# Kernel tuning notes

Measured on AMD Instinct MI355X. Metric: run time of the kernel, lower is better.

Reference implementation:

```python
import jax, jax.numpy as jnp
import numpy as np

S, B, T = 128, 1024, 96
E, H, HH, ATT = 64, 200, 100, 200
ACT, FLD = 32, 8
V_SRC, N_PROD, V_PRIM, N_FLD = 20000, 101, 10000, 64
DEC_IN = ACT + ATT + FLD + H  # 440


def setup_inputs() -> dict:
    key = jax.random.key(0)
    ks = jax.random.split(key, 24)
    rn = lambda k, shp: jax.random.normal(k, shp, dtype=jnp.float32) * 0.05
    sentences = jax.random.randint(ks[0], (S, B), 0, V_SRC)
    is_prod = jax.random.randint(ks[1], (T, B), 0, 2).astype(jnp.int32)
    prod_ids = jax.random.randint(ks[2], (T, B), 0, N_PROD)
    prim_ids = jax.random.randint(ks[3], (T, B), 0, V_PRIM)
    field_ids = jax.random.randint(ks[4], (T, B), 0, N_FLD)
    pt = jax.random.randint(ks[5], (T, B), 0, T)
    parent_t = jnp.minimum(pt, jnp.maximum(jnp.arange(T)[:, None] - 1, 0))  # parent < t
    return {
        'sentences': sentences, 'is_prod': is_prod, 'prod_ids': prod_ids,
        'prim_ids': prim_ids, 'field_ids': field_ids, 'parent_t': parent_t,
        'src_emb': rn(ks[6], (V_SRC, E)),
        'actprod_emb': rn(ks[7], (N_PROD, ACT)),
        'prim_emb': rn(ks[8], (V_PRIM, ACT)),
        'field_emb': rn(ks[9], (N_FLD, FLD)),
        'Wih_f': rn(ks[10], (4 * HH, E)), 'Whh_f': rn(ks[11], (4 * HH, HH)), 'b_f': rn(ks[12], (4 * HH,)),
        'Wih_b': rn(ks[13], (4 * HH, E)), 'Whh_b': rn(ks[14], (4 * HH, HH)), 'b_b': rn(ks[15], (4 * HH,)),
        'Wih_d': rn(ks[16], (4 * H, DEC_IN)), 'Whh_d': rn(ks[17], (4 * H, H)), 'b_d': rn(ks[18], (4 * H,)),
        'W_attn': rn(ks[19], (H, H)),
        'W_av': rn(ks[20], (ATT, 2 * H)),
    }


def _lstm_cell(z, c):
    i, f, g, o = jnp.split(z, 4, axis=-1)  # torch gate order i,f,g,o
    c = jax.nn.sigmoid(f) * c + jax.nn.sigmoid(i) * jnp.tanh(g)
    h = jax.nn.sigmoid(o) * jnp.tanh(c)
    return h, c


def _lstm_dir(x_emb, Wih, Whh, b, reverse):
    # x_emb: [S,B,E]; precompute input projections once
    xw = jnp.einsum('sbe,he->sbh', x_emb, Wih) + b
    nb = x_emb.shape[1]
    hh = Whh.shape[1]
    init = (jnp.zeros((nb, hh), x_emb.dtype), jnp.zeros((nb, hh), x_emb.dtype))
    def step(carry, xw_t):
        h, c = carry
        h, c = _lstm_cell(xw_t + h @ Whh.T, c)
        return (h, c), h
    (hT, cT), hs = jax.lax.scan(step, init, xw, reverse=reverse)
    return hs, hT, cT


def _forward(sentences, is_prod, prod_ids, prim_ids, field_ids, parent_t,
             src_emb, actprod_emb, prim_emb, field_emb,
             Wih_f, Whh_f, b_f, Wih_b, Whh_b, b_b,
             Wih_d, Whh_d, b_d, W_attn, W_av):
    nb = sentences.shape[1]
    nt = is_prod.shape[0]
    emb = src_emb[sentences]                       # [S,B,E]
    hs_f, hTf, cTf = _lstm_dir(emb, Wih_f, Whh_f, b_f, False)
    hs_b, hTb, cTb = _lstm_dir(emb, Wih_b, Whh_b, b_b, True)
    enc = jnp.concatenate([hs_f, hs_b], -1).transpose(1, 0, 2)   # [B,S,H]
    enc_att = enc @ W_attn.T                                     # [B,S,H]
    # replicate torch h0.view(-1, H) on [2,B,HH]
    h = jnp.stack([hTf, hTb]).reshape(-1, H)
    c = jnp.stack([cTf, cTb]).reshape(-1, H)
    Hbuf = jnp.zeros((nt, nb, H), enc.dtype)
    s_att0 = jnp.zeros((nb, ATT), enc.dtype)
    barange = jnp.arange(nb)

    def dec_step(carry, xs):
        h, c, s_att, Hbuf = carry
        t, ip, pid, prid, fid, ptid = xs
        a_tm1 = jnp.where(ip[:, None] == 1, actprod_emb[pid], prim_emb[prid])  # [B,32]
        nft = field_emb[fid]                                                   # [B,8]
        parent = Hbuf[ptid, barange]                                           # [B,H] irregular gather
        inp = jnp.concatenate([a_tm1, s_att, nft, parent], axis=-1)           # [B,440]
        inp = jnp.where(t > 0, inp, jnp.zeros_like(inp))
        h, c = _lstm_cell(inp @ Wih_d.T + h @ Whh_d.T + b_d, c)
        aw = jax.nn.softmax(jnp.einsum('bsh,bh->bs', enc_att, h), axis=-1)
        ctx = jnp.einsum('bs,bsh->bh', aw, enc)
        s_att = jnp.tanh(jnp.concatenate([ctx, h], axis=1) @ W_av.T)
        Hbuf = Hbuf.at[t].set(h)
        return (h, c, s_att, Hbuf), s_att

    xs = (jnp.arange(nt), is_prod, prod_ids, prim_ids, field_ids, parent_t)
    _, att_vecs = jax.lax.scan(dec_step, (h, c, s_att0, Hbuf), xs)
    return att_vecs  # [T,B,ATT]


def reference(sentences, is_prod, prod_ids, prim_ids, field_ids, parent_t,
              src_emb, actprod_emb, prim_emb, field_emb,
              Wih_f, Whh_f, b_f, Wih_b, Whh_b, b_b,
              Wih_d, Whh_d, b_d, W_attn, W_av):
    return _forward(sentences, is_prod, prod_ids, prim_ids, field_ids, parent_t,
                    src_emb, actprod_emb, prim_emb, field_emb,
                    Wih_f, Whh_f, b_f, Wih_b, Whh_b, b_b,
                    Wih_d, Whh_d, b_d, W_attn, W_av)
```

## Files before the change

### kernel.cpp

```cpp
#include <hip/hip_runtime.h>

#define S_LEN 128
#define B_N   1024
#define T_LEN 96
#define E_DIM 64
#define HH    100
#define H_DIM 200
#define ACT_D 32
#define FLD_D 8
#define ATT_D 200
#define DEC_IN 440
#define KTOT  640
#define G4H   800
#define G4HH  400
#define KH_PAD 224
#define KC_PAD 416
#define NCOL_PAD 208
#define EK_ROWS 208
#define XA_LD 648
#define HG_LD 232
#define CAT_LD 424

typedef unsigned int  u32;
typedef unsigned short u16;
typedef _Float16 f16;
typedef _Float16 f16x8 __attribute__((ext_vector_type(8)));
typedef _Float16 f16x4 __attribute__((ext_vector_type(4)));
typedef float    f32x4 __attribute__((ext_vector_type(4)));

#define MFMA16(a,b,c) __builtin_amdgcn_mfma_f32_16x16x32_f16((a),(b),(c),0,0,0)

static __device__ __forceinline__ float lo_bf(u32 u){ union{u32 i; float f;}v; v.i = u<<16; return v.f; }
static __device__ __forceinline__ float hi_bf(u32 u){ union{u32 i; float f;}v; v.i = u & 0xffff0000u; return v.f; }
static __device__ __forceinline__ float sigf(float x){
  x = fminf(30.f, fmaxf(-30.f, x));
  return 1.f/(1.f + __expf(-x));
}
static __device__ __forceinline__ float tanhf_(float x){
  x = fminf(15.f, fmaxf(-15.f, x));
  float e = __expf(-2.f*x);
  return (1.f - e)/(1.f + e);
}

static __device__ __forceinline__ u16 f2bf(float f){
  union{float f; u32 i;} v; v.f = f;
  u32 r = v.i + 0x7fffu + ((v.i >> 16) & 1u);
  return (u16)(r >> 16);
}
__global__ void k_prep(u16* __restrict__ dst, const float* __restrict__ src,
                       int K, int C, int sk, int sc)
{
  int idx = blockIdx.x*256 + threadIdx.x;
  if (idx >= K*C) return;
  int k = idx / C, c = idx - k*C;
  dst[(size_t)(k>>2)*(4*C) + 4*c + (k&3)] = f2bf(src[(size_t)k*sk + (size_t)c*sc]);
}

__global__ void k_pack16(f16* __restrict__ dst, const float* __restrict__ src,
                         int Kld, int koff, int C, int K, int sk, int sc)
{
  int idx = blockIdx.x*256 + threadIdx.x;
  if (idx >= C*K) return;
  int c = idx / K, k = idx - c*K;
  dst[(size_t)c*Kld + koff + k] = (f16)src[(size_t)k*sk + (size_t)c*sc];
}

__global__ void k_zf16(f16* __restrict__ dst, int n)
{
  int idx = blockIdx.x*256 + threadIdx.x;
  if (idx < n) dst[idx] = (f16)0.f;
}

__global__ __launch_bounds__(256) void k_transpose(
    const f16* __restrict__ enc_sk, f16* __restrict__ enc_ks)
{
  __shared__ f16 ld[H_DIM][136];
  const int b = blockIdx.x, tid = threadIdx.x;
  const f16* src = enc_sk + (size_t)b*S_LEN*H_DIM;
  for (int idx = tid; idx < S_LEN*(H_DIM/4); idx += 256) {
    int s = idx / (H_DIM/4), jc = idx - s*(H_DIM/4);
    f16x4 v = *(const f16x4*)(src + (size_t)s*H_DIM + 4*jc);
    #pragma unroll
    for (int i = 0; i < 4; ++i) ld[4*jc + i][s] = v[i];
  }
  __syncthreads();
  f16* dst = enc_ks + (size_t)b*EK_ROWS*S_LEN;
  for (int idx = tid; idx < H_DIM*(S_LEN/8); idx += 256) {
    int k = idx / (S_LEN/8), so = idx - k*(S_LEN/8);
    f16x8 v;
    #pragma unroll
    for (int i = 0; i < 8; ++i) v[i] = ld[k][8*so + i];
    *(f16x8*)(dst + (size_t)k*S_LEN + 8*so) = v;
  }
}

__global__ __launch_bounds__(512) void k_attgemm(
    const f16* __restrict__ enc_sk, const f16* __restrict__ wattnT,
    f16* __restrict__ enc_att)
{
  __shared__ alignas(16) f16 et[S_LEN][KH_PAD];
  const int b = blockIdx.x, tid = threadIdx.x;
  const int lane = tid & 63, wid = tid >> 6;
  const int arow = lane & 15, aoff = (lane >> 4) * 8;
  const f16* src = enc_sk + (size_t)b*S_LEN*H_DIM;
  for (int idx = tid; idx < S_LEN*(H_DIM/8); idx += 512) {
    int s = idx / (H_DIM/8), jo = idx - s*(H_DIM/8);
    *(f16x8*)&et[s][8*jo] = *(const f16x8*)(src + (size_t)s*H_DIM + 8*jo);
  }
  for (int idx = tid; idx < S_LEN*3; idx += 512) {
    int s = idx / 3, jo = idx - s*3;
    *(f16x8*)&et[s][H_DIM + 8*jo] = (f16x8){0,0,0,0,0,0,0,0};
  }
  __syncthreads();
  f16x8 af[7];
  #pragma unroll
  for (int kk = 0; kk < 7; ++kk)
    af[kk] = *(const f16x8*)&et[wid*16 + arow][kk*32 + aoff];
  f16* dstb = enc_att + (size_t)b*EK_ROWS*S_LEN;
  for (int tt = 0; tt < 13; ++tt) {
    int c = tt*16 + arow;
    f32x4 acc = {0.f,0.f,0.f,0.f};
    const f16* p = wattnT + (size_t)c*KH_PAD + aoff;
    #pragma unroll
    for (int kk = 0; kk < 7; ++kk)
      acc = MFMA16(af[kk], *(const f16x8*)(p + kk*32), acc);
    int srow = wid*16 + (lane >> 4)*4;
    f16x4 v;
    #pragma unroll
    for (int i = 0; i < 4; ++i) v[i] = (f16)acc[i];
    *(f16x4*)(dstb + (size_t)c*S_LEN + srow) = v;
  }
}

__global__ __launch_bounds__(512) void k_encoder(
    const int* __restrict__ sentences, const float* __restrict__ src_emb,
    const float* __restrict__ b_f, const float* __restrict__ b_b,
    const uint2* __restrict__ wihF, const uint2* __restrict__ whhF,
    const uint2* __restrict__ wihB, const uint2* __restrict__ whhB,
    f16* __restrict__ enc_sk,
    float* __restrict__ hTf, float* __restrict__ cTf,
    float* __restrict__ hTb, float* __restrict__ cTb)
{
  const int tid = threadIdx.x;
  const int dir = blockIdx.x >> 7;
  const int bg  = blockIdx.x & 127;
  const int b0  = bg * 8;

  __shared__ alignas(16) float xs[8][E_DIM];
  __shared__ alignas(16) float hs[8][HH];
  __shared__ alignas(16) float zs[8][G4HH];

  const uint2* wih = dir ? wihB : wihF;
  const uint2* whh = dir ? whhB : whhF;
  const float* bias = dir ? b_b : b_f;

  for (int idx = tid; idx < 8*HH; idx += 512) ((float*)hs)[idx] = 0.f;
  float c0r = 0.f, c1r = 0.f;

  const int col = tid;
  const bool act = (col < G4HH);
  const float bias0 = act ? bias[col] : 0.f;

  __syncthreads();

  for (int step = 0; step < S_LEN; ++step) {
    const int s = dir ? (S_LEN-1-step) : step;
    {
      int r = tid >> 6, e = tid & 63;
      int tok = sentences[s*B_N + (b0 + r)];
      xs[r][e] = src_emb[(size_t)tok*E_DIM + e];
    }
    __syncthreads();

    if (act) {
      float acc[8];
      #pragma unroll
      for (int r = 0; r < 8; ++r) acc[r] = bias0;
      #pragma unroll 2
      for (int k4 = 0; k4 < E_DIM/4; ++k4) {
        uint2 u = wih[k4*G4HH + col];
        float w0 = lo_bf(u.x), w1 = hi_bf(u.x), w2 = lo_bf(u.y), w3 = hi_bf(u.y);
        #pragma unroll
        for (int r = 0; r < 8; ++r) {
          float4 xv = *(const float4*)&xs[r][4*k4];
          acc[r] += xv.x*w0 + xv.y*w1 + xv.z*w2 + xv.w*w3;
        }
      }
      #pragma unroll 2
      for (int k4 = 0; k4 < HH/4; ++k4) {
        uint2 u = whh[k4*G4HH + col];
        float w0 = lo_bf(u.x), w1 = hi_bf(u.x), w2 = lo_bf(u.y), w3 = hi_bf(u.y);
        #pragma unroll
        for (int r = 0; r < 8; ++r) {
          float4 hv = *(const float4*)&hs[r][4*k4];
          acc[r] += hv.x*w0 + hv.y*w1 + hv.z*w2 + hv.w*w3;
        }
      }
      #pragma unroll
      for (int r = 0; r < 8; ++r) zs[r][col] = acc[r];
    }
    __syncthreads();

    {
      int r = tid / HH, j = tid - r*HH;
      float c = sigf(zs[r][HH+j])*c0r + sigf(zs[r][j])*tanhf_(zs[r][2*HH+j]);
      float h = sigf(zs[r][3*HH+j])*tanhf_(c);
      c0r = c;
      hs[r][j] = h;
      enc_sk[((size_t)(b0+r)*S_LEN + s)*H_DIM + dir*HH + j] = (f16)h;
      if (tid < 8*HH - 512) {
        int idx2 = tid + 512;
        int r2 = idx2 / HH, j2 = idx2 - r2*HH;
        float c2 = sigf(zs[r2][HH+j2])*c1r + sigf(zs[r2][j2])*tanhf_(zs[r2][2*HH+j2]);
        float h2 = sigf(zs[r2][3*HH+j2])*tanhf_(c2);
        c1r = c2;
        hs[r2][j2] = h2;
        enc_sk[((size_t)(b0+r2)*S_LEN + s)*H_DIM + dir*HH + j2] = (f16)h2;
      }
    }
    __syncthreads();
  }

  float* hT = dir ? hTb : hTf;
  float* cT = dir ? cTb : cTf;
  {
    int r = tid / HH, j = tid - r*HH;
    hT[(b0+r)*HH + j] = hs[r][j];
    cT[(b0+r)*HH + j] = c0r;
    if (tid < 8*HH - 512) {
      int idx2 = tid + 512; int r2 = idx2 / HH, j2 = idx2 - r2*HH;
      hT[(b0+r2)*HH + j2] = hs[r2][j2];
      cT[(b0+r2)*HH + j2] = c1r;
    }
  }
}

__global__ __launch_bounds__(512, 2) void k_decoder(
  const int* __restrict__ is_prod, const int* __restrict__ prod_ids,
  const int* __restrict__ prim_ids, const int* __restrict__ field_ids,
  const int* __restrict__ parent_t,
  const float* __restrict__ actprod_emb, const float* __restrict__ prim_emb,
  const float* __restrict__ field_emb, const float* __restrict__ b_d,
  const f16* __restrict__ wall,
  const f16* __restrict__ wav,
  const f16* __restrict__ enc_ks,
  const f16* __restrict__ enc_att,
  const float* __restrict__ hTf, const float* __restrict__ cTf,
  const float* __restrict__ hTb, const float* __restrict__ cTb,
  f16* __restrict__ Hbuf, float* __restrict__ out)
{
  const int tid  = threadIdx.x;
  const int lane = tid & 63;
  const int wid  = tid >> 6;
  const int b0   = blockIdx.x * 4;
  const int arow = lane & 15;
  const int aoff = (lane >> 4) * 8;

  __shared__ alignas(16) f16   xa[4][XA_LD];
  __shared__ alignas(16) f16   hg[4][HG_LD];
  __shared__ alignas(16) f16   cat[4][CAT_LD];
  __shared__ alignas(16) f16   aw_sh[4][S_LEN];
  __shared__ alignas(16) float zs[4][G4H];
  __shared__ float biasd[G4H];

  for (int idx = tid; idx < G4H; idx += 512) biasd[idx] = b_d[idx];
  for (int idx = tid; idx < 4*(HG_LD-H_DIM); idx += 512) {
    int n = HG_LD-H_DIM; hg[idx/n][H_DIM + idx%n] = (f16)0.f;
  }
  for (int idx = tid; idx < 4*(CAT_LD-2*H_DIM); idx += 512) {
    int n = CAT_LD-2*H_DIM; cat[idx/n][2*H_DIM + idx%n] = (f16)0.f;
  }
  for (int idx = tid; idx < 4*DEC_IN; idx += 512) {
    xa[idx/DEC_IN][idx%DEC_IN] = (f16)0.f;
  }
  for (int idx = tid; idx < 4*H_DIM; idx += 512) {
    int r = idx / H_DIM, j = idx - r*H_DIM; int b = b0 + r;
    float v;
    if (b < 512) v = (j < HH) ? hTf[(2*b)*HH + j] : hTf[(2*b+1)*HH + (j-HH)];
    else { int bb = b-512; v = (j < HH) ? hTb[(2*bb)*HH + j] : hTb[(2*bb+1)*HH + (j-HH)]; }
    f16 hv = (f16)v;
    xa[r][DEC_IN + j] = hv; hg[r][j] = hv; cat[r][H_DIM + j] = hv;
  }
  float cst[2] = {0.f, 0.f};
  #pragma unroll
  for (int kk = 0; kk < 2; ++kk) {
    int slot = tid + 512*kk;
    if (slot < 4*H_DIM) {
      int r = slot / H_DIM, j = slot - r*H_DIM; int b = b0 + r;
      float v;
      if (b < 512) v = (j < HH) ? cTf[(2*b)*HH + j] : cTf[(2*b+1)*HH + (j-HH)];
      else { int bb = b-512; v = (j < HH) ? cTb[(2*bb)*HH + j] : cTb[(2*bb+1)*HH + (j-HH)]; }
      cst[kk] = v;
    }
  }
  __syncthreads();

  for (int t = 0; t < T_LEN; ++t) {
    {
      f16x8 afr[20];
      #pragma unroll
      for (int kk = 0; kk < 20; ++kk) {
        f16x8 v = {0,0,0,0,0,0,0,0};
        if (arow < 4) v = *(const f16x8*)&xa[arow][kk*32 + aoff];
        afr[kk] = v;
      }
      for (int tt = wid; tt < 50; tt += 8) {
        int c = tt*16 + arow;
        float bv = biasd[c];
        f32x4 acc = {bv, bv, bv, bv};
        const f16* p = wall + (size_t)c*KTOT + aoff;
        #pragma unroll
        for (int kk = 0; kk < 20; ++kk)
          acc = MFMA16(afr[kk], *(const f16x8*)(p + kk*32), acc);
        if (lane < 16) {
          #pragma unroll
          for (int i2 = 0; i2 < 4; ++i2) zs[i2][c] = acc[i2];
        }
      }
    }
    __syncthreads();

    #pragma unroll
    for (int kk = 0; kk < 2; ++kk) {
      int slot = tid + 512*kk;
      if (slot < 4*H_DIM) {
        int r = slot / H_DIM, j = slot - r*H_DIM;
        float c = sigf(zs[r][H_DIM+j])*cst[kk] + sigf(zs[r][j])*tanhf_(zs[r][2*H_DIM+j]);
        float h = sigf(zs[r][3*H_DIM+j])*tanhf_(c);
        cst[kk] = c;
        f16 hv = (f16)h;
        xa[r][DEC_IN + j] = hv; hg[r][j] = hv; cat[r][H_DIM + j] = hv;
        Hbuf[((size_t)t*B_N + (b0+r))*H_DIM + j] = hv;
      }
    }
    __syncthreads();

    if (wid < 4) {
      const int r = wid;
      const int sl = lane & 15, kp = lane >> 4;
      const f16* ep = enc_att + ((size_t)(b0+r)*EK_ROWS + kp*52)*S_LEN + 8*sl;
      const f16* hp = &hg[r][kp*52];
      float acc[8] = {0.f,0.f,0.f,0.f,0.f,0.f,0.f,0.f};
      #pragma unroll 4
      for (int i = 0; i < 52; ++i) {
        f16x8 e8 = *(const f16x8*)(ep + (size_t)i*S_LEN);
        float hf = (float)hp[i];
        #pragma unroll
        for (int q = 0; q < 8; ++q) acc[q] += hf * (float)e8[q];
      }
      #pragma unroll
      for (int q = 0; q < 8; ++q) {
        acc[q] += __shfl_xor(acc[q], 16);
        acc[q] += __shfl_xor(acc[q], 32);
      }
      float m = acc[0];
      #pragma unroll
      for (int q = 1; q < 8; ++q) m = fmaxf(m, acc[q]);
      #pragma unroll
      for (int d = 1; d < 16; d <<= 1) m = fmaxf(m, __shfl_xor(m, d));
      float e[8], sm = 0.f;
      #pragma unroll
      for (int q = 0; q < 8; ++q) { e[q] = __expf(acc[q] - m); sm += e[q]; }
      #pragma unroll
      for (int d = 1; d < 16; d <<= 1) sm += __shfl_xor(sm, d);
      float rd = 1.f / sm;
      if (kp == 0) {
        f16x8 w;
        #pragma unroll
        for (int q = 0; q < 8; ++q) w[q] = (f16)(e[q] * rd);
        *(f16x8*)&aw_sh[r][8*sl] = w;
      }
    }
    __syncthreads();

    {
      #pragma unroll
      for (int pass = 0; pass < 2; ++pass) {
        int tt = wid + pass*8;
        if (tt < 13) {
          int c = tt*16 + arow;
          f32x4 acc = {0.f,0.f,0.f,0.f};
          const f16* eb = enc_ks + (size_t)b0*EK_ROWS*S_LEN + (size_t)c*S_LEN + aoff;
          #pragma unroll 4
          for (int kt = 0; kt < 16; ++kt) {
            int rp = kt >> 2;
            int s0 = (kt & 3) * 32;
            f16x8 a = {0,0,0,0,0,0,0,0};
            if (arow == rp) a = *(const f16x8*)&aw_sh[rp][s0 + aoff];
            f16x8 bf = *(const f16x8*)(eb + (size_t)rp*EK_ROWS*S_LEN + s0);
            acc = MFMA16(a, bf, acc);
          }
          if (lane < 16 && c < H_DIM) {
            #pragma unroll
            for (int i2 = 0; i2 < 4; ++i2) cat[i2][c] = (f16)acc[i2];
          }
        }
      }
      if (t + 1 < T_LEN) {
        const int tn = t + 1;
        for (int idx = tid; idx < 4*DEC_IN; idx += 512) {
          int r = idx / DEC_IN, k = idx - r*DEC_IN;
          if (k >= ACT_D && k < ACT_D + ATT_D) continue;
          int b = b0 + r;
          f16 v;
          if (k < ACT_D) {
            float f = (is_prod[tn*B_N + b] == 1)
              ? actprod_emb[prod_ids[tn*B_N + b]*ACT_D + k]
              : prim_emb[prim_ids[tn*B_N + b]*ACT_D + k];
            v = (f16)f;
          } else if (k < ACT_D + ATT_D + FLD_D) {
            v = (f16)field_emb[field_ids[tn*B_N + b]*FLD_D + (k - ACT_D - ATT_D)];
          } else {
            int pt = parent_t[tn*B_N + b];
            v = Hbuf[((size_t)pt*B_N + b)*H_DIM + (k - (ACT_D+ATT_D+FLD_D))];
          }
          xa[r][k] = v;
        }
      }
    }
    __syncthreads();

    {
      f16x8 sa[13];
      #pragma unroll
      for (int kk = 0; kk < 13; ++kk) {
        f16x8 v = {0,0,0,0,0,0,0,0};
        if (arow < 4) v = *(const f16x8*)&cat[arow][kk*32 + aoff];
        sa[kk] = v;
      }
      #pragma unroll
      for (int pass = 0; pass < 2; ++pass) {
        int tt = wid + pass*8;
        if (tt < 13) {
          int c = tt*16 + arow;
          f32x4 acc = {0.f,0.f,0.f,0.f};
          const f16* p = wav + (size_t)c*KC_PAD + aoff;
          #pragma unroll
          for (int kk = 0; kk < 13; ++kk)
            acc = MFMA16(sa[kk], *(const f16x8*)(p + kk*32), acc);
          if (lane < 16 && c < ATT_D) {
            #pragma unroll
            for (int i2 = 0; i2 < 4; ++i2) {
              float v = tanhf_(acc[i2]);
              out[((size_t)t*B_N + (b0+i2))*ATT_D + c] = v;
              xa[i2][ACT_D + c] = (f16)v;
            }
          }
        }
      }
    }
    __syncthreads();
  }
}

extern "C" void kernel_launch(void* const* d_in, const int* in_sizes, int n_in,
                              void* d_out, int out_size, void* d_ws, size_t ws_size,
                              hipStream_t stream)
{
  const int*   sentences = (const int*)  d_in[0];
  const int*   is_prod   = (const int*)  d_in[1];
  const int*   prod_ids  = (const int*)  d_in[2];
  const int*   prim_ids  = (const int*)  d_in[3];
  const int*   field_ids = (const int*)  d_in[4];
  const int*   parent_t  = (const int*)  d_in[5];
  const float* src_emb   = (const float*)d_in[6];
  const float* actprod   = (const float*)d_in[7];
  const float* prim_emb  = (const float*)d_in[8];
  const float* field_emb = (const float*)d_in[9];
  const float* Wih_f = (const float*)d_in[10];
  const float* Whh_f = (const float*)d_in[11];
  const float* b_f   = (const float*)d_in[12];
  const float* Wih_b = (const float*)d_in[13];
  const float* Whh_b = (const float*)d_in[14];
  const float* b_b   = (const float*)d_in[15];
  const float* Wih_d = (const float*)d_in[16];
  const float* Whh_d = (const float*)d_in[17];
  const float* b_d   = (const float*)d_in[18];
  const float* W_attn= (const float*)d_in[19];
  const float* W_av  = (const float*)d_in[20];
  (void)in_sizes; (void)n_in; (void)out_size; (void)ws_size;

  char* ws = (char*)d_ws;
  size_t off = 0;
  auto take = [&](size_t bytes) -> void* {
    void* p = ws + off;
    off = (off + bytes + 255) & ~(size_t)255;
    return p;
  };
  u16* wihF = (u16*)take((size_t)64*400*2);
  u16* whhF = (u16*)take((size_t)100*400*2);
  u16* wihB = (u16*)take((size_t)64*400*2);
  u16* whhB = (u16*)take((size_t)100*400*2);
  f16* wall16  = (f16*)take((size_t)800*640*2);
  f16* wattnT  = (f16*)take((size_t)NCOL_PAD*KH_PAD*2);
  f16* wav16   = (f16*)take((size_t)NCOL_PAD*KC_PAD*2);
  f16* enc_sk  = (f16*)take((size_t)B_N*S_LEN*H_DIM*2);
  f16* enc_ks  = (f16*)take((size_t)B_N*EK_ROWS*S_LEN*2);
  f16* enc_att = (f16*)take((size_t)B_N*EK_ROWS*S_LEN*2);
  float* hTf = (float*)take((size_t)B_N*HH*4);
  float* cTf = (float*)take((size_t)B_N*HH*4);
  float* hTb = (float*)take((size_t)B_N*HH*4);
  float* cTb = (float*)take((size_t)B_N*HH*4);
  f16* Hbuf16 = (f16*)take((size_t)T_LEN*B_N*H_DIM*2);
  float* outp = (float*)d_out;

  auto prep = [&](u16* dst, const float* src, int K, int C, int sk, int sc){
    int n = K*C;
    k_prep<<<(n+255)/256, 256, 0, stream>>>(dst, src, K, C, sk, sc);
  };
  prep(wihF, Wih_f, 64, 400, 1, 64);
  prep(whhF, Whh_f, 100, 400, 1, 100);
  prep(wihB, Wih_b, 64, 400, 1, 64);
  prep(whhB, Whh_b, 100, 400, 1, 100);

  {
    int n;
    n = NCOL_PAD*KH_PAD; k_zf16<<<(n+255)/256,256,0,stream>>>(wattnT, n);
    n = NCOL_PAD*KC_PAD; k_zf16<<<(n+255)/256,256,0,stream>>>(wav16, n);
    n = 800*440; k_pack16<<<(n+255)/256,256,0,stream>>>(wall16, Wih_d, KTOT, 0,   800, 440, 1, 440);
    n = 800*200; k_pack16<<<(n+255)/256,256,0,stream>>>(wall16, Whh_d, KTOT, 440, 800, 200, 1, 200);
    n = 200*200; k_pack16<<<(n+255)/256,256,0,stream>>>(wattnT, W_attn, KH_PAD, 0, 200, 200, 1, 200);
    n = 200*400; k_pack16<<<(n+255)/256,256,0,stream>>>(wav16, W_av, KC_PAD, 0, 200, 400, 1, 400);
  }

  k_encoder<<<256, 512, 0, stream>>>(sentences, src_emb, b_f, b_b,
      (const uint2*)wihF, (const uint2*)whhF, (const uint2*)wihB, (const uint2*)whhB,
      enc_sk, hTf, cTf, hTb, cTb);

  k_transpose<<<B_N, 256, 0, stream>>>(enc_sk, enc_ks);
  k_attgemm<<<B_N, 512, 0, stream>>>(enc_sk, wattnT, enc_att);

  k_decoder<<<256, 512, 0, stream>>>(is_prod, prod_ids, prim_ids, field_ids, parent_t,
      actprod, prim_emb, field_emb, b_d,
      wall16, wav16,
      enc_ks, enc_att, hTf, cTf, hTb, cTb, Hbuf16, outp);
}
```

Measured before the change: 6.673 ms.

## Apply W_attn to decoder state per step and keep encoder tile in LDS

Drops the precomputed enc_att tensor and the k_attgemm kernel. Each decoder step instead projects h through W_attn with MFMA (g = W_attn^T h) and scores against the raw encoder outputs. The transposed encoder slice for each batch row is cached in shared memory for the whole decoder loop, and the batch per block falls from 4 to 2 to fit it (512 blocks). This removes a large global intermediate and the repeated global reads of encoder data each step, at the cost of an extra small GEMM per step, heavy LDS use, and lower MFMA row utilisation (2 of 16 rows).

```diff
diff --git a/kernel.cpp b/kernel.cpp
--- a/kernel.cpp
+++ b/kernel.cpp
@@ -17,9 +17,12 @@
 #define KC_PAD 416
 #define NCOL_PAD 208
 #define EK_ROWS 208
+#define EK_SLD 136
 #define XA_LD 648
 #define HG_LD 232
+#define GA_LD 232
 #define CAT_LD 424
+#define ROWS 2
 
 typedef unsigned int  u32;
 typedef unsigned short u16;
@@ -91,44 +94,6 @@
     #pragma unroll
     for (int i = 0; i < 8; ++i) v[i] = ld[k][8*so + i];
     *(f16x8*)(dst + (size_t)k*S_LEN + 8*so) = v;
-  }
-}
-
-__global__ __launch_bounds__(512) void k_attgemm(
-    const f16* __restrict__ enc_sk, const f16* __restrict__ wattnT,
-    f16* __restrict__ enc_att)
-{
-  __shared__ alignas(16) f16 et[S_LEN][KH_PAD];
-  const int b = blockIdx.x, tid = threadIdx.x;
-  const int lane = tid & 63, wid = tid >> 6;
-  const int arow = lane & 15, aoff = (lane >> 4) * 8;
-  const f16* src = enc_sk + (size_t)b*S_LEN*H_DIM;
-  for (int idx = tid; idx < S_LEN*(H_DIM/8); idx += 512) {
-    int s = idx / (H_DIM/8), jo = idx - s*(H_DIM/8);
-    *(f16x8*)&et[s][8*jo] = *(const f16x8*)(src + (size_t)s*H_DIM + 8*jo);
-  }
-  for (int idx = tid; idx < S_LEN*3; idx += 512) {
-    int s = idx / 3, jo = idx - s*3;
-    *(f16x8*)&et[s][H_DIM + 8*jo] = (f16x8){0,0,0,0,0,0,0,0};
-  }
-  __syncthreads();
-  f16x8 af[7];
-  #pragma unroll
-  for (int kk = 0; kk < 7; ++kk)
-    af[kk] = *(const f16x8*)&et[wid*16 + arow][kk*32 + aoff];
-  f16* dstb = enc_att + (size_t)b*EK_ROWS*S_LEN;
-  for (int tt = 0; tt < 13; ++tt) {
-    int c = tt*16 + arow;
-    f32x4 acc = {0.f,0.f,0.f,0.f};
-    const f16* p = wattnT + (size_t)c*KH_PAD + aoff;
-    #pragma unroll
-    for (int kk = 0; kk < 7; ++kk)
-      acc = MFMA16(af[kk], *(const f16x8*)(p + kk*32), acc);
-    int srow = wid*16 + (lane >> 4)*4;
-    f16x4 v;
-    #pragma unroll
-    for (int i = 0; i < 4; ++i) v[i] = (f16)acc[i];
-    *(f16x4*)(dstb + (size_t)c*S_LEN + srow) = v;
   }
 }
 
@@ -242,9 +207,9 @@
   const float* __restrict__ actprod_emb, const float* __restrict__ prim_emb,
   const float* __restrict__ field_emb, const float* __restrict__ b_d,
   const f16* __restrict__ wall,
+  const f16* __restrict__ wattn,
   const f16* __restrict__ wav,
   const f16* __restrict__ enc_ks,
-  const f16* __restrict__ enc_att,
   const float* __restrict__ hTf, const float* __restrict__ cTf,
   const float* __restrict__ hTb, const float* __restrict__ cTb,
   f16* __restrict__ Hbuf, float* __restrict__ out)
@@ -252,28 +217,40 @@
   const int tid  = threadIdx.x;
   const int lane = tid & 63;
   const int wid  = tid >> 6;
-  const int b0   = blockIdx.x * 4;
+  const int b0   = blockIdx.x * ROWS;
   const int arow = lane & 15;
   const int aoff = (lane >> 4) * 8;
 
-  __shared__ alignas(16) f16   xa[4][XA_LD];
-  __shared__ alignas(16) f16   hg[4][HG_LD];
-  __shared__ alignas(16) f16   cat[4][CAT_LD];
-  __shared__ alignas(16) f16   aw_sh[4][S_LEN];
-  __shared__ alignas(16) float zs[4][G4H];
+  __shared__ alignas(16) f16   encl[ROWS][H_DIM][EK_SLD];
+  __shared__ alignas(16) f16   xa[ROWS][XA_LD];
+  __shared__ alignas(16) f16   hg[ROWS][HG_LD];
+  __shared__ alignas(16) f16   gA[ROWS][GA_LD];
+  __shared__ alignas(16) f16   cat[ROWS][CAT_LD];
+  __shared__ alignas(16) f16   aw_sh[ROWS][S_LEN];
+  __shared__ alignas(16) float zs[ROWS][G4H];
   __shared__ float biasd[G4H];
 
   for (int idx = tid; idx < G4H; idx += 512) biasd[idx] = b_d[idx];
-  for (int idx = tid; idx < 4*(HG_LD-H_DIM); idx += 512) {
+  for (int idx = tid; idx < ROWS*(HG_LD-H_DIM); idx += 512) {
     int n = HG_LD-H_DIM; hg[idx/n][H_DIM + idx%n] = (f16)0.f;
   }
-  for (int idx = tid; idx < 4*(CAT_LD-2*H_DIM); idx += 512) {
+  for (int idx = tid; idx < ROWS*(GA_LD-H_DIM); idx += 512) {
+    int n = GA_LD-H_DIM; gA[idx/n][H_DIM + idx%n] = (f16)0.f;
+  }
+  for (int idx = tid; idx < ROWS*(CAT_LD-2*H_DIM); idx += 512) {
     int n = CAT_LD-2*H_DIM; cat[idx/n][2*H_DIM + idx%n] = (f16)0.f;
   }
-  for (int idx = tid; idx < 4*DEC_IN; idx += 512) {
+  for (int idx = tid; idx < ROWS*DEC_IN; idx += 512) {
     xa[idx/DEC_IN][idx%DEC_IN] = (f16)0.f;
   }
-  for (int idx = tid; idx < 4*H_DIM; idx += 512) {
+  for (int idx = tid; idx < ROWS*H_DIM*(S_LEN/8); idx += 512) {
+    int r  = idx / (H_DIM*(S_LEN/8));
+    int rm = idx - r*(H_DIM*(S_LEN/8));
+    int k  = rm / (S_LEN/8), so = rm - k*(S_LEN/8);
+    *(f16x8*)&encl[r][k][8*so] =
+      *(const f16x8*)(enc_ks + ((size_t)(b0+r)*EK_ROWS + k)*S_LEN + 8*so);
+  }
+  for (int idx = tid; idx < ROWS*H_DIM; idx += 512) {
     int r = idx / H_DIM, j = idx - r*H_DIM; int b = b0 + r;
     float v;
     if (b < 512) v = (j < HH) ? hTf[(2*b)*HH + j] : hTf[(2*b+1)*HH + (j-HH)];
@@ -281,17 +258,11 @@
     f16 hv = (f16)v;
     xa[r][DEC_IN + j] = hv; hg[r][j] = hv; cat[r][H_DIM + j] = hv;
   }
-  float cst[2] = {0.f, 0.f};
-  #pragma unroll
-  for (int kk = 0; kk < 2; ++kk) {
-    int slot = tid + 512*kk;
-    if (slot < 4*H_DIM) {
-      int r = slot / H_DIM, j = slot - r*H_DIM; int b = b0 + r;
-      float v;
-      if (b < 512) v = (j < HH) ? cTf[(2*b)*HH + j] : cTf[(2*b+1)*HH + (j-HH)];
-      else { int bb = b-512; v = (j < HH) ? cTb[(2*bb)*HH + j] : cTb[(2*bb+1)*HH + (j-HH)]; }
-      cst[kk] = v;
-    }
+  float cst = 0.f;
+  if (tid < ROWS*H_DIM) {
+    int r = tid / H_DIM, j = tid - r*H_DIM; int b = b0 + r;
+    if (b < 512) cst = (j < HH) ? cTf[(2*b)*HH + j] : cTf[(2*b+1)*HH + (j-HH)];
+    else { int bb = b-512; cst = (j < HH) ? cTb[(2*bb)*HH + j] : cTb[(2*bb+1)*HH + (j-HH)]; }
   }
   __syncthreads();
 
@@ -301,7 +272,7 @@
       #pragma unroll
       for (int kk = 0; kk < 20; ++kk) {
         f16x8 v = {0,0,0,0,0,0,0,0};
-        if (arow < 4) v = *(const f16x8*)&xa[arow][kk*32 + aoff];
+        if (arow < ROWS) v = *(const f16x8*)&xa[arow][kk*32 + aoff];
         afr[kk] = v;
       }
       for (int tt = wid; tt < 50; tt += 8) {
@@ -314,39 +285,61 @@
           acc = MFMA16(afr[kk], *(const f16x8*)(p + kk*32), acc);
         if (lane < 16) {
           #pragma unroll
-          for (int i2 = 0; i2 < 4; ++i2) zs[i2][c] = acc[i2];
-        }
-      }
-    }
-    __syncthreads();
-
-    #pragma unroll
-    for (int kk = 0; kk < 2; ++kk) {
-      int slot = tid + 512*kk;
-      if (slot < 4*H_DIM) {
-        int r = slot / H_DIM, j = slot - r*H_DIM;
-        float c = sigf(zs[r][H_DIM+j])*cst[kk] + sigf(zs[r][j])*tanhf_(zs[r][2*H_DIM+j]);
-        float h = sigf(zs[r][3*H_DIM+j])*tanhf_(c);
-        cst[kk] = c;
-        f16 hv = (f16)h;
-        xa[r][DEC_IN + j] = hv; hg[r][j] = hv; cat[r][H_DIM + j] = hv;
-        Hbuf[((size_t)t*B_N + (b0+r))*H_DIM + j] = hv;
-      }
-    }
-    __syncthreads();
-
-    if (wid < 4) {
+          for (int i2 = 0; i2 < ROWS; ++i2) zs[i2][c] = acc[i2];
+        }
+      }
+    }
+    __syncthreads();
+
+    if (tid < ROWS*H_DIM) {
+      int r = tid / H_DIM, j = tid - r*H_DIM;
+      float c = sigf(zs[r][H_DIM+j])*cst + sigf(zs[r][j])*tanhf_(zs[r][2*H_DIM+j]);
+      float h = sigf(zs[r][3*H_DIM+j])*tanhf_(c);
+      cst = c;
+      f16 hv = (f16)h;
+      xa[r][DEC_IN + j] = hv; hg[r][j] = hv; cat[r][H_DIM + j] = hv;
+      Hbuf[((size_t)t*B_N + (b0+r))*H_DIM + j] = hv;
+    }
+    __syncthreads();
+
+    {
+      f16x8 ga[7];
+      #pragma unroll
+      for (int kk = 0; kk < 7; ++kk) {
+        f16x8 v = {0,0,0,0,0,0,0,0};
+        if (arow < ROWS) v = *(const f16x8*)&hg[arow][kk*32 + aoff];
+        ga[kk] = v;
+      }
+      #pragma unroll
+      for (int pass = 0; pass < 2; ++pass) {
+        int tt = wid + pass*8;
+        if (tt < 13) {
+          int c = tt*16 + arow;
+          f32x4 acc = {0.f,0.f,0.f,0.f};
+          const f16* p = wattn + (size_t)c*KH_PAD + aoff;
+          #pragma unroll
+          for (int kk = 0; kk < 7; ++kk)
+            acc = MFMA16(ga[kk], *(const f16x8*)(p + kk*32), acc);
+          if (lane < 16 && c < H_DIM) {
+            #pragma unroll
+            for (int i2 = 0; i2 < ROWS; ++i2) gA[i2][c] = (f16)acc[i2];
+          }
+        }
+      }
+    }
+    __syncthreads();
+
+    if (wid < ROWS) {
       const int r = wid;
       const int sl = lane & 15, kp = lane >> 4;
-      const f16* ep = enc_att + ((size_t)(b0+r)*EK_ROWS + kp*52)*S_LEN + 8*sl;
-      const f16* hp = &hg[r][kp*52];
       float acc[8] = {0.f,0.f,0.f,0.f,0.f,0.f,0.f,0.f};
-      #pragma unroll 4
-      for (int i = 0; i < 52; ++i) {
-        f16x8 e8 = *(const f16x8*)(ep + (size_t)i*S_LEN);
-        float hf = (float)hp[i];
+      #pragma unroll 5
+      for (int i = 0; i < 50; ++i) {
+        int k = kp*50 + i;
+        f16x8 e8 = *(const f16x8*)&encl[r][k][8*sl];
+        float gf = (float)gA[r][k];
         #pragma unroll
-        for (int q = 0; q < 8; ++q) acc[q] += hf * (float)e8[q];
+        for (int q = 0; q < 8; ++q) acc[q] += gf * (float)e8[q];
       }
       #pragma unroll
       for (int q = 0; q < 8; ++q) {
@@ -380,25 +373,25 @@
         if (tt < 13) {
           int c = tt*16 + arow;
           f32x4 acc = {0.f,0.f,0.f,0.f};
-          const f16* eb = enc_ks + (size_t)b0*EK_ROWS*S_LEN + (size_t)c*S_LEN + aoff;
-          #pragma unroll 4
-          for (int kt = 0; kt < 16; ++kt) {
+          #pragma unroll
+          for (int kt = 0; kt < 4*ROWS; ++kt) {
             int rp = kt >> 2;
             int s0 = (kt & 3) * 32;
             f16x8 a = {0,0,0,0,0,0,0,0};
             if (arow == rp) a = *(const f16x8*)&aw_sh[rp][s0 + aoff];
-            f16x8 bf = *(const f16x8*)(eb + (size_t)rp*EK_ROWS*S_LEN + s0);
+            f16x8 bf = {0,0,0,0,0,0,0,0};
+            if (c < H_DIM) bf = *(const f16x8*)&encl[rp][c][s0 + aoff];
             acc = MFMA16(a, bf, acc);
           }
           if (lane < 16 && c < H_DIM) {
             #pragma unroll
-            for (int i2 = 0; i2 < 4; ++i2) cat[i2][c] = (f16)acc[i2];
+            for (int i2 = 0; i2 < ROWS; ++i2) cat[i2][c] = (f16)acc[i2];
           }
         }
       }
       if (t + 1 < T_LEN) {
         const int tn = t + 1;
-        for (int idx = tid; idx < 4*DEC_IN; idx += 512) {
+        for (int idx = tid; idx < ROWS*DEC_IN; idx += 512) {
           int r = idx / DEC_IN, k = idx - r*DEC_IN;
           if (k >= ACT_D && k < ACT_D + ATT_D) continue;
           int b = b0 + r;
@@ -425,7 +418,7 @@
       #pragma unroll
       for (int kk = 0; kk < 13; ++kk) {
         f16x8 v = {0,0,0,0,0,0,0,0};
-        if (arow < 4) v = *(const f16x8*)&cat[arow][kk*32 + aoff];
+        if (arow < ROWS) v = *(const f16x8*)&cat[arow][kk*32 + aoff];
         sa[kk] = v;
       }
       #pragma unroll
@@ -440,7 +433,7 @@
             acc = MFMA16(sa[kk], *(const f16x8*)(p + kk*32), acc);
           if (lane < 16 && c < ATT_D) {
             #pragma unroll
-            for (int i2 = 0; i2 < 4; ++i2) {
+            for (int i2 = 0; i2 < ROWS; ++i2) {
               float v = tanhf_(acc[i2]);
               out[((size_t)t*B_N + (b0+i2))*ATT_D + c] = v;
               xa[i2][ACT_D + c] = (f16)v;
@@ -492,11 +485,10 @@
   u16* wihB = (u16*)take((size_t)64*400*2);
   u16* whhB = (u16*)take((size_t)100*400*2);
   f16* wall16  = (f16*)take((size_t)800*640*2);
-  f16* wattnT  = (f16*)take((size_t)NCOL_PAD*KH_PAD*2);
+  f16* wattn16 = (f16*)take((size_t)NCOL_PAD*KH_PAD*2);
   f16* wav16   = (f16*)take((size_t)NCOL_PAD*KC_PAD*2);
   f16* enc_sk  = (f16*)take((size_t)B_N*S_LEN*H_DIM*2);
   f16* enc_ks  = (f16*)take((size_t)B_N*EK_ROWS*S_LEN*2);
-  f16* enc_att = (f16*)take((size_t)B_N*EK_ROWS*S_LEN*2);
   float* hTf = (float*)take((size_t)B_N*HH*4);
   float* cTf = (float*)take((size_t)B_N*HH*4);
   float* hTb = (float*)take((size_t)B_N*HH*4);
@@ -515,11 +507,11 @@
 
   {
     int n;
-    n = NCOL_PAD*KH_PAD; k_zf16<<<(n+255)/256,256,0,stream>>>(wattnT, n);
+    n = NCOL_PAD*KH_PAD; k_zf16<<<(n+255)/256,256,0,stream>>>(wattn16, n);
     n = NCOL_PAD*KC_PAD; k_zf16<<<(n+255)/256,256,0,stream>>>(wav16, n);
     n = 800*440; k_pack16<<<(n+255)/256,256,0,stream>>>(wall16, Wih_d, KTOT, 0,   800, 440, 1, 440);
     n = 800*200; k_pack16<<<(n+255)/256,256,0,stream>>>(wall16, Whh_d, KTOT, 440, 800, 200, 1, 200);
-    n = 200*200; k_pack16<<<(n+255)/256,256,0,stream>>>(wattnT, W_attn, KH_PAD, 0, 200, 200, 1, 200);
+    n = 200*200; k_pack16<<<(n+255)/256,256,0,stream>>>(wattn16, W_attn, KH_PAD, 0, 200, 200, 200, 1);
     n = 200*400; k_pack16<<<(n+255)/256,256,0,stream>>>(wav16, W_av, KC_PAD, 0, 200, 400, 1, 400);
   }
 
@@ -528,10 +520,9 @@
       enc_sk, hTf, cTf, hTb, cTb);
 
   k_transpose<<<B_N, 256, 0, stream>>>(enc_sk, enc_ks);
-  k_attgemm<<<B_N, 512, 0, stream>>>(enc_sk, wattnT, enc_att);
-
-  k_decoder<<<256, 512, 0, stream>>>(is_prod, prod_ids, prim_ids, field_ids, parent_t,
+
+  k_decoder<<<B_N/ROWS, 512, 0, stream>>>(is_prod, prod_ids, prim_ids, field_ids, parent_t,
       actprod, prim_emb, field_emb, b_d,
-      wall16, wav16,
-      enc_ks, enc_att, hTf, cTf, hTb, cTb, Hbuf16, outp);
-}
+      wall16, wattn16, wav16,
+      enc_ks, hTf, cTf, hTb, cTb, Hbuf16, outp);
+}
```

After: 8.769 ms. +31.4%, slower.
